# Kernel optimization log

Measured on AMD Instinct MI355X. Metric: run time of the kernel, lower is better.

The kernel has to match this reference:

```python
import jax, jax.numpy as jnp
import numpy as np

EMB = 2048
N_HEADS = 16
HEAD_DIM = EMB // N_HEADS
ROPE_BASE = 10000.0


def _rope_cos_sin(seq_len, head_dim, dtype):
    inv_freq = 1.0 / (ROPE_BASE ** (jnp.arange(0, head_dim, 2, dtype=jnp.float32) / head_dim))
    t = jnp.arange(seq_len, dtype=jnp.float32)
    freqs = jnp.einsum('s,d->sd', t, inv_freq)          # [S, head_dim/2]
    emb = jnp.concatenate([freqs, freqs], axis=-1)       # [S, head_dim]
    return jnp.cos(emb).astype(dtype), jnp.sin(emb).astype(dtype)


def _rotate_half(x):
    x1, x2 = jnp.split(x, 2, axis=-1)
    return jnp.concatenate([-x2, x1], axis=-1)


def _apply_rope(x, cos, sin):
    # x: [B, H, S, D]; cos/sin: [S, D]
    return x * cos[None, None, :, :] + _rotate_half(x) * sin[None, None, :, :]


def setup_inputs() -> dict:
    key = jax.random.key(0)
    k1, k2, k3 = jax.random.split(key, 3)
    B, S = 4, 2048
    x = jax.random.normal(k1, (B, S, EMB), dtype=jnp.float32)
    # Additive causal mask: 0 on/below diagonal, -1e9 above.
    causal = jnp.triu(jnp.full((S, S), -1e9, dtype=jnp.float32), k=1)
    att_mask = causal[None, None, :, :]
    Wqkv = jax.random.normal(k2, (3 * EMB, EMB), dtype=jnp.float32) * (EMB ** -0.5)
    Wout = jax.random.normal(k3, (EMB, EMB), dtype=jnp.float32) * (EMB ** -0.5)
    return {"x": x, "att_mask": att_mask, "Wqkv": Wqkv, "Wout": Wout}


def reference(x, att_mask, Wqkv, Wout):
    B, S, E = x.shape
    qkv = jnp.einsum('bse,fe->bsf', x, Wqkv)             # [B, S, 3E]
    q, k, v = jnp.split(qkv, 3, axis=-1)
    def to_heads(t):
        return t.reshape(B, S, N_HEADS, HEAD_DIM).transpose(0, 2, 1, 3)  # [B,H,S,D]
    q, k, v = to_heads(q), to_heads(k), to_heads(v)
    cos, sin = _rope_cos_sin(S, HEAD_DIM, x.dtype)
    q = _apply_rope(q, cos, sin)
    k = _apply_rope(k, cos, sin)
    scaling = HEAD_DIM ** -0.5
    dots = jnp.einsum('bhqd,bhkd->bhqk', q, k) * scaling
    dots = dots + att_mask
    attn = jax.nn.softmax(dots, axis=-1)
    out = jnp.einsum('bhqk,bhkd->bhqd', attn, v)         # [B,H,S,D]
    out = out.transpose(0, 2, 1, 3).reshape(B, S, E)
    return jnp.einsum('bse,fe->bsf', out, Wout)
```

## Files before the change

### kernel.cpp

```cpp
#include <hip/hip_runtime.h>
#include <stdint.h>

typedef __attribute__((ext_vector_type(8))) short short8_t;
typedef __attribute__((ext_vector_type(4))) float f32x4;

__device__ __forceinline__ short f2bf(float f) {
  union { float f; uint32_t u; } v; v.f = f;
  uint32_t r = v.u + 0x7FFFu + ((v.u >> 16) & 1u);
  return (short)(r >> 16);
}
__device__ __forceinline__ float bf2f(short s) {
  union { uint32_t u; float f; } v; v.u = ((uint32_t)(uint16_t)s) << 16; return v.f;
}
__device__ __forceinline__ void gld16(const void* g, void* l) {
  __builtin_amdgcn_global_load_lds((const __attribute__((address_space(1))) void*)g,
                                   (__attribute__((address_space(3))) void*)l, 16, 0, 0);
}

__global__ __launch_bounds__(256) void conv_kernel(const float* __restrict__ in,
                                                   short* __restrict__ out, int n4) {
  int i = blockIdx.x * 256 + threadIdx.x;
  const int stride = gridDim.x * 256;
  for (; i < n4; i += stride) {
    float4 v = reinterpret_cast<const float4*>(in)[i];
    short4 o;
    o.x = f2bf(v.x); o.y = f2bf(v.y); o.z = f2bf(v.z); o.w = f2bf(v.w);
    reinterpret_cast<short4*>(out)[i] = o;
  }
}

__device__ __forceinline__ void storeC(float* C, size_t i, float v) { C[i] = v; }
__device__ __forceinline__ void storeC(short* C, size_t i, float v) { C[i] = f2bf(v); }

template <typename OT>
__global__ __launch_bounds__(512, 2) void gemm8p(const short* __restrict__ A,
                                                 const short* __restrict__ B,
                                                 OT* __restrict__ C, int M, int N, int K,
                                                 int nbx) {
  __shared__ __align__(16) short lds[65536];
  const int tid = threadIdx.x, lane = tid & 63, w = tid >> 6;
  const int wr = w >> 2, wc = w & 3;
  const int c = lane & 15, g4 = lane >> 4;
  const int lin = (blockIdx.x & 7) * ((int)gridDim.x >> 3) + ((int)blockIdx.x >> 3);
  const int bx = lin % nbx, by = lin / nbx;
  const size_t m0 = (size_t)by * 256, n0 = (size_t)bx * 256;
  const size_t Kb = (size_t)K * 2;
  const char* Ab = (const char*)A + m0 * Kb;
  const char* Bb = (const char*)B + n0 * Kb;
  const char* aq[2];
  const char* bq[2];
#pragma unroll
  for (int i = 0; i < 2; ++i) {
    const size_t ro = (size_t)((i * 8 + w) * 16 + c) * Kb + g4 * 16;
    aq[i] = Ab + ro;
    bq[i] = Bb + ro;
  }
  char* alds = (char*)lds;
  const int aoff = wr * 8192 + lane * 16;
  const int boff = 65536 + wc * 4096 + lane * 16;
  f32x4 acc[8][4] = {};
  const int NT = K >> 6, NIT = NT >> 1;

#define STAGE(q, srcoff, ldsbase)                                  \
  gld16((q)[0] + (srcoff), alds + (ldsbase) + (w << 10));          \
  gld16((q)[1] + (srcoff), alds + (ldsbase) + ((8 + w) << 10))

  STAGE(aq, 0, 0);
  STAGE(bq, 0, 65536);
  STAGE(aq, 64, 16384);
  STAGE(bq, 64, 81920);
  STAGE(aq, 128, 32768);
  STAGE(bq, 128, 98304);
  asm volatile("s_waitcnt vmcnt(0)" ::: "memory");
  asm volatile("s_barrier" ::: "memory");

  short8_t af[4], bfr[4];

#define RD_A(mi, OFF) \
  asm volatile("ds_read_b128 %0, %1 offset:%c2" : "=v"(af[mi]) : "v"(aoff), "i"(OFF))
#define RD_B(ni, OFF) \
  asm volatile("ds_read_b128 %0, %1 offset:%c2" : "=v"(bfr[ni]) : "v"(boff), "i"(OFF))

#define MFMA16(MQ)                                                                       \
  __builtin_amdgcn_s_setprio(1);                                                         \
  _Pragma("unroll") for (int mi = 0; mi < 4; ++mi) {                                     \
    _Pragma("unroll") for (int n = 0; n < 4; ++n)                                        \
      acc[(MQ)*4 + mi][n] =                                                              \
          __builtin_amdgcn_mfma_f32_16x16x32_bf16(af[mi], bfr[n], acc[(MQ)*4 + mi][n],   \
                                                  0, 0, 0);                              \
  }                                                                                      \
  __builtin_amdgcn_s_setprio(0)

#define PH_EVEN(BSEL, KS, q, srcoff, sbase)                        \
  RD_B(0, (BSEL) + (KS)*16384 + 0);                                \
  RD_B(1, (BSEL) + (KS)*16384 + 1024);                             \
  RD_B(2, (BSEL) + (KS)*16384 + 2048);                             \
  RD_B(3, (BSEL) + (KS)*16384 + 3072);                             \
  RD_A(0, (BSEL) + (KS)*16384 + 0 * 1024);                         \
  RD_A(1, (BSEL) + (KS)*16384 + 1 * 1024);                         \
  RD_A(2, (BSEL) + (KS)*16384 + 2 * 1024);                         \
  RD_A(3, (BSEL) + (KS)*16384 + 3 * 1024);                         \
  STAGE(q, srcoff, sbase);                                         \
  asm volatile("s_barrier" ::: "memory");                          \
  asm volatile("s_waitcnt lgkmcnt(0)" ::: "memory");               \
  __builtin_amdgcn_sched_barrier(0);                               \
  MFMA16(0);                                                       \
  asm volatile("s_barrier" ::: "memory")

#define PH_ODD(BSEL, KS, q, srcoff, sbase)                         \
  RD_A(0, (BSEL) + (KS)*16384 + 4 * 1024);                         \
  RD_A(1, (BSEL) + (KS)*16384 + 5 * 1024);                         \
  RD_A(2, (BSEL) + (KS)*16384 + 6 * 1024);                         \
  RD_A(3, (BSEL) + (KS)*16384 + 7 * 1024);                         \
  STAGE(q, srcoff, sbase);                                         \
  asm volatile("s_barrier" ::: "memory");                          \
  asm volatile("s_waitcnt lgkmcnt(0)" ::: "memory");               \
  __builtin_amdgcn_sched_barrier(0);                               \
  MFMA16(1);                                                       \
  asm volatile("s_waitcnt vmcnt(8)" ::: "memory");                 \
  asm volatile("s_barrier" ::: "memory")

  for (int it = 0; it < NIT; ++it) {
    const int T = it << 1;
    const int t1 = (T + 1) << 7;
    const int t2 = (T + 2 < NT ? T + 2 : NT - 1) << 7;
    const int t3 = (T + 3 < NT ? T + 3 : NT - 1) << 7;
    PH_EVEN(0, 0, aq, t1 + 64, 49152);
    PH_ODD (0, 0, bq, t1 + 64, 114688);
    PH_EVEN(0, 1, aq, t2, 0);
    PH_ODD (0, 1, bq, t2, 65536);
    PH_EVEN(32768, 0, aq, t2 + 64, 16384);
    PH_ODD (32768, 0, bq, t2 + 64, 81920);
    PH_EVEN(32768, 1, aq, t3, 32768);
    PH_ODD (32768, 1, bq, t3, 98304);
  }
#undef PH_EVEN
#undef PH_ODD
#undef MFMA16
#undef RD_A
#undef RD_B
#undef STAGE

#pragma unroll
  for (int m = 0; m < 8; ++m)
#pragma unroll
    for (int n = 0; n < 4; ++n) {
      const size_t col = n0 + wc * 64 + n * 16 + c;
      const size_t rb = m0 + wr * 128 + m * 16 + g4 * 4;
#pragma unroll
      for (int r = 0; r < 4; ++r) storeC(C, (rb + r) * (size_t)N + col, acc[m][n][r]);
    }
}

__global__ __launch_bounds__(256) void rope_kernel(short* __restrict__ qkv) {
  const int g = blockIdx.x * 256 + threadIdx.x;
  const int jg = g & 7;
  const int h = (g >> 3) & 15;
  const int bs = g >> 7;
  const int s = bs & 2047;
  const size_t base = (size_t)bs * 6144 + 2048 + h * 128 + jg * 8;
  short8_t lo = *(short8_t*)&qkv[base];
  short8_t hi = *(short8_t*)&qkv[base + 64];
  short8_t olo, ohi;
#pragma unroll
  for (int t = 0; t < 8; ++t) {
    const int j = jg * 8 + t;
    const float inv = exp2f((float)j * -0.20762050593046f);
    float sn, cn;
    sincosf((float)s * inv, &sn, &cn);
    const float a = bf2f(lo[t]), b = bf2f(hi[t]);
    olo[t] = f2bf(a * cn - b * sn);
    ohi[t] = f2bf(b * cn + a * sn);
  }
  *(short8_t*)&qkv[base] = olo;
  *(short8_t*)&qkv[base + 64] = ohi;
}

__global__ __launch_bounds__(256) void vt_kernel(const short* __restrict__ qkv,
                                                 short* __restrict__ vt) {
  __shared__ __align__(16) short Vl[64][128];
  const int g = blockIdx.x;
  const int st = g & 31, bh = g >> 5;
  const int h = bh & 15, b = bh >> 4;
  const int t = threadIdx.x;
  const int s0 = st * 64;
#pragma unroll
  for (int p = 0; p < 4; ++p) {
    const int idx = p * 256 + t;
    const int row = idx >> 4, c16 = idx & 15;
    short8_t v = *(const short8_t*)&qkv[(size_t)(b * 2048 + s0 + row) * 6144 + 4096 + h * 128 + c16 * 8];
    *(short8_t*)&Vl[row][c16 * 8] = v;
  }
  __syncthreads();
  const size_t obase = ((size_t)(b * 16 + h) * 128) * 2048;
#pragma unroll
  for (int i = 0; i < 8; ++i) {
    const int idx = t * 8 + i;
    const int d = idx >> 4, sq = idx & 15;
    short4 o;
    o.x = Vl[sq * 4 + 0][d];
    o.y = Vl[sq * 4 + 1][d];
    o.z = Vl[sq * 4 + 2][d];
    o.w = Vl[sq * 4 + 3][d];
    *(short4*)&vt[obase + (size_t)d * 2048 + s0 + sq * 4] = o;
  }
}

__global__ __launch_bounds__(256) void attn_kernel(const short* __restrict__ qkv,
                                                   const short* __restrict__ vt,
                                                   short* __restrict__ o) {
  __shared__ __align__(16) short Kl[2][64 * 128];
  __shared__ __align__(16) short Vl[2][128 * 64];
  __shared__ __align__(16) short Pl[4][16 * 72];
  const int tid = threadIdx.x, lane = tid & 63, w = tid >> 6;
  const int c = lane & 15, g4 = lane >> 4;
  const int blk = blockIdx.x;
  const int xcd = blk & 7;
  const int l = blk >> 3;
  const int bh = xcd * 8 + (l >> 5);
  const int h = bh & 15, b = bh >> 4;
  const int q0 = (31 - (l & 31)) * 64;
  const int srow = q0 + w * 16 + c;

  short8_t qf[4];
  {
    const size_t qr = ((size_t)b * 2048 + srow) * 6144 + h * 128;
    float fl[4][8];
#pragma unroll
    for (int dc = 0; dc < 4; ++dc) {
      short8_t rawv = *(const short8_t*)&qkv[qr + dc * 32 + g4 * 8];
#pragma unroll
      for (int t = 0; t < 8; ++t) fl[dc][t] = bf2f(rawv[t]);
    }
#pragma unroll
    for (int pd = 0; pd < 2; ++pd)
#pragma unroll
      for (int t = 0; t < 8; ++t) {
        const int j = pd * 32 + g4 * 8 + t;
        const float inv = exp2f((float)j * -0.20762050593046f);
        float sn, cn;
        sincosf((float)srow * inv, &sn, &cn);
        const float a = fl[pd][t], bb = fl[pd + 2][t];
        fl[pd][t] = a * cn - bb * sn;
        fl[pd + 2][t] = bb * cn + a * sn;
      }
#pragma unroll
    for (int dc = 0; dc < 4; ++dc) {
      short8_t q8;
#pragma unroll
      for (int t = 0; t < 8; ++t) q8[t] = f2bf(fl[dc][t]);
      qf[dc] = q8;
    }
  }

  f32x4 acc_o[8] = {};
  float rs[4] = {0.f, 0.f, 0.f, 0.f};
  const float scale2 = 0.12751875222364685f;
  const char* Kbase = (const char*)qkv + ((size_t)b * 2048 * 6144 + 2048 + h * 128) * 2;
  const char* Vbase = (const char*)vt + ((size_t)(b * 16 + h) * 128 * 2048) * 2;

  const char* kq[4];
  const char* vq[4];
#pragma unroll
  for (int i = 0; i < 4; ++i) {
    const int L = ((w * 4 + i) << 10) + lane * 16;
    {
      const int row = L >> 8, inner = L & 255;
      kq[i] = Kbase + (size_t)row * 12288 + (inner ^ ((row & 7) << 4));
    }
    {
      const int row = L >> 7, inner = L & 127;
      vq[i] = Vbase + (size_t)row * 4096 + (inner ^ ((row & 7) << 4));
    }
  }
  auto stage = [&](int buf, int kv0) {
#pragma unroll
    for (int i = 0; i < 4; ++i) {
      gld16(kq[i] + (size_t)kv0 * 12288, (char*)Kl + (buf << 14) + ((w * 4 + i) << 10));
      gld16(vq[i] + (size_t)kv0 * 2, (char*)Vl + (buf << 14) + ((w * 4 + i) << 10));
    }
  };

  stage(0, 0);
  __syncthreads();
  int cur = 0;
  for (int kv0 = 0; kv0 <= q0; kv0 += 64) {
    if (kv0 + 64 <= q0) stage(cur ^ 1, kv0 + 64);
    const char* Kb = (const char*)Kl + (cur << 14);
    const char* Vb = (const char*)Vl + (cur << 14);
    const bool diag = (kv0 == q0);
    float p[4][4];
#pragma unroll
    for (int kt = 0; kt < 4; ++kt) {
      f32x4 s4 = {};
      const int krow = kt * 16 + c;
      __builtin_amdgcn_s_setprio(1);
#pragma unroll
      for (int dc = 0; dc < 4; ++dc) {
        const int inner = (dc * 64 + g4 * 16) ^ ((krow & 7) << 4);
        short8_t kf = *(const short8_t*)(Kb + krow * 256 + inner);
        s4 = __builtin_amdgcn_mfma_f32_16x16x32_bf16(qf[dc], kf, s4, 0, 0, 0);
      }
      __builtin_amdgcn_s_setprio(0);
#pragma unroll
      for (int r = 0; r < 4; ++r) {
        float v = s4[r] * scale2 - 8.0f;
        if (diag) {
          const int kc = kv0 + kt * 16 + c;
          const int qr2 = q0 + w * 16 + g4 * 4 + r;
          if (kc > qr2) v = -1e30f;
        }
        const float pe = exp2f(v);
        p[kt][r] = pe;
        rs[r] += pe;
      }
    }
#pragma unroll
    for (int kt = 0; kt < 4; ++kt)
#pragma unroll
      for (int r = 0; r < 4; r += 2) {
        uint32_t pk;
        asm("v_cvt_pk_bf16_f32 %0, %1, %2" : "=v"(pk) : "v"(p[kt][r]), "v"(p[kt][r + 1]));
        Pl[w][(g4 * 4 + r) * 72 + kt * 16 + c] = (short)(pk & 0xffffu);
        Pl[w][(g4 * 4 + r + 1) * 72 + kt * 16 + c] = (short)(pk >> 16);
      }
#pragma unroll
    for (int kk = 0; kk < 2; ++kk) {
      short8_t pf = *(const short8_t*)&Pl[w][c * 72 + kk * 32 + g4 * 8];
      __builtin_amdgcn_s_setprio(1);
#pragma unroll
      for (int dt = 0; dt < 8; ++dt) {
        const int vrow = dt * 16 + c;
        const int inner = (kk * 64 + g4 * 16) ^ ((vrow & 7) << 4);
        short8_t vf = *(const short8_t*)(Vb + vrow * 128 + inner);
        acc_o[dt] = __builtin_amdgcn_mfma_f32_16x16x32_bf16(pf, vf, acc_o[dt], 0, 0, 0);
      }
      __builtin_amdgcn_s_setprio(0);
    }
    __syncthreads();
    cur ^= 1;
  }
#pragma unroll
  for (int off = 1; off < 16; off <<= 1)
#pragma unroll
    for (int r = 0; r < 4; ++r) rs[r] += __shfl_xor(rs[r], off);
  const size_t ob = ((size_t)b * 2048 + q0 + w * 16 + g4 * 4) * 2048 + h * 128;
#pragma unroll
  for (int dt = 0; dt < 8; ++dt)
#pragma unroll
    for (int r = 0; r < 4; ++r)
      o[ob + (size_t)r * 2048 + dt * 16 + c] = f2bf(acc_o[dt][r] / rs[r]);
}

extern "C" void kernel_launch(void* const* d_in, const int* in_sizes, int n_in,
                              void* d_out, int out_size, void* d_ws, size_t ws_size,
                              hipStream_t stream) {
  const float* x = (const float*)d_in[0];
  const float* Wqkv = (const float*)d_in[2];
  const float* Wout = (const float*)d_in[3];
  float* out = (float*)d_out;
  char* ws = (char*)d_ws;
  short* xb   = (short*)ws;
  short* wqb  = (short*)(ws + 33554432ull);
  short* qkv  = (short*)(ws + 58720256ull);
  short* vt   = (short*)(ws + 159383552ull);
  short* attno = xb;
  short* woutb = wqb;

  conv_kernel<<<2048, 256, 0, stream>>>(x, xb, 16777216 / 4);
  conv_kernel<<<2048, 256, 0, stream>>>(Wqkv, wqb, 12582912 / 4);
  gemm8p<short><<<768, 512, 0, stream>>>(xb, wqb, qkv, 8192, 6144, 2048, 24);
  conv_kernel<<<2048, 256, 0, stream>>>(Wout, woutb, 4194304 / 4);
  rope_kernel<<<4096, 256, 0, stream>>>(qkv);
  vt_kernel<<<2048, 256, 0, stream>>>(qkv, vt);
  attn_kernel<<<2048, 256, 0, stream>>>(qkv, vt, attno);
  gemm8p<float><<<256, 512, 0, stream>>>(attno, woutb, out, 8192, 2048, 2048, 8);
}
```

Measured before the change: 535.9 us.

## Double-buffer LDS fragment registers to prefetch next phase during MFMA

Adds two register sets for the A and B fragments in the GEMM main loop. Each phase now issues the LDS reads for the next phase before running its own MFMAs, and waits only on partial lgkmcnt counts. One barrier per phase is removed. The aim is to hide LDS read latency behind matrix math, at the cost of more VGPRs and tighter correctness requirements on the waitcnt/barrier ordering against async global-to-LDS staging.

```diff
diff --git a/kernel.cpp b/kernel.cpp
--- a/kernel.cpp
+++ b/kernel.cpp
@@ -61,6 +61,8 @@
   f32x4 acc[8][4] = {};
   const int NT = K >> 6, NIT = NT >> 1;
 
+  short8_t af[2][4], bfr[2][4];
+
 #define STAGE(q, srcoff, ldsbase)                                  \
   gld16((q)[0] + (srcoff), alds + (ldsbase) + (w << 10));          \
   gld16((q)[1] + (srcoff), alds + (ldsbase) + ((8 + w) << 10))
@@ -74,69 +76,73 @@
   asm volatile("s_waitcnt vmcnt(0)" ::: "memory");
   asm volatile("s_barrier" ::: "memory");
 
-  short8_t af[4], bfr[4];
-
-#define RD_A(mi, OFF) \
-  asm volatile("ds_read_b128 %0, %1 offset:%c2" : "=v"(af[mi]) : "v"(aoff), "i"(OFF))
-#define RD_B(ni, OFF) \
-  asm volatile("ds_read_b128 %0, %1 offset:%c2" : "=v"(bfr[ni]) : "v"(boff), "i"(OFF))
-
-#define MFMA16(MQ)                                                                       \
+#define RD_A(S, mi, OFF) \
+  asm volatile("ds_read_b128 %0, %1 offset:%c2" : "=v"(af[S][mi]) : "v"(aoff), "i"(OFF))
+#define RD_B(S, ni, OFF) \
+  asm volatile("ds_read_b128 %0, %1 offset:%c2" : "=v"(bfr[S][ni]) : "v"(boff), "i"(OFF))
+
+#define PREF_A(S, BSEL, KS, MQ)                           \
+  RD_A(S, 0, (BSEL) + (KS)*16384 + ((MQ)*4 + 0) * 1024);  \
+  RD_A(S, 1, (BSEL) + (KS)*16384 + ((MQ)*4 + 1) * 1024);  \
+  RD_A(S, 2, (BSEL) + (KS)*16384 + ((MQ)*4 + 2) * 1024);  \
+  RD_A(S, 3, (BSEL) + (KS)*16384 + ((MQ)*4 + 3) * 1024)
+
+#define PREF_B(S, BSEL, KS)                  \
+  RD_B(S, 0, (BSEL) + (KS)*16384 + 0);       \
+  RD_B(S, 1, (BSEL) + (KS)*16384 + 1024);    \
+  RD_B(S, 2, (BSEL) + (KS)*16384 + 2048);    \
+  RD_B(S, 3, (BSEL) + (KS)*16384 + 3072)
+
+#define MFMA16(AS, BS, MQ)                                                               \
   __builtin_amdgcn_s_setprio(1);                                                         \
   _Pragma("unroll") for (int mi = 0; mi < 4; ++mi) {                                     \
     _Pragma("unroll") for (int n = 0; n < 4; ++n)                                        \
-      acc[(MQ)*4 + mi][n] =                                                              \
-          __builtin_amdgcn_mfma_f32_16x16x32_bf16(af[mi], bfr[n], acc[(MQ)*4 + mi][n],   \
-                                                  0, 0, 0);                              \
+      acc[(MQ)*4 + mi][n] = __builtin_amdgcn_mfma_f32_16x16x32_bf16(                     \
+          af[AS][mi], bfr[BS][n], acc[(MQ)*4 + mi][n], 0, 0, 0);                         \
   }                                                                                      \
   __builtin_amdgcn_s_setprio(0)
 
-#define PH_EVEN(BSEL, KS, q, srcoff, sbase)                        \
-  RD_B(0, (BSEL) + (KS)*16384 + 0);                                \
-  RD_B(1, (BSEL) + (KS)*16384 + 1024);                             \
-  RD_B(2, (BSEL) + (KS)*16384 + 2048);                             \
-  RD_B(3, (BSEL) + (KS)*16384 + 3072);                             \
-  RD_A(0, (BSEL) + (KS)*16384 + 0 * 1024);                         \
-  RD_A(1, (BSEL) + (KS)*16384 + 1 * 1024);                         \
-  RD_A(2, (BSEL) + (KS)*16384 + 2 * 1024);                         \
-  RD_A(3, (BSEL) + (KS)*16384 + 3 * 1024);                         \
+#define PHASE_E(AS, BS, PBSEL, PKS, q, srcoff, sbase)              \
+  PREF_A(AS ^ 1, PBSEL, PKS, 1);                                   \
   STAGE(q, srcoff, sbase);                                         \
-  asm volatile("s_barrier" ::: "memory");                          \
-  asm volatile("s_waitcnt lgkmcnt(0)" ::: "memory");               \
+  asm volatile("s_waitcnt lgkmcnt(4)" ::: "memory");               \
   __builtin_amdgcn_sched_barrier(0);                               \
-  MFMA16(0);                                                       \
+  MFMA16(AS, BS, 0);                                               \
+  asm volatile("s_waitcnt vmcnt(6)" ::: "memory");                 \
   asm volatile("s_barrier" ::: "memory")
 
-#define PH_ODD(BSEL, KS, q, srcoff, sbase)                         \
-  RD_A(0, (BSEL) + (KS)*16384 + 4 * 1024);                         \
-  RD_A(1, (BSEL) + (KS)*16384 + 5 * 1024);                         \
-  RD_A(2, (BSEL) + (KS)*16384 + 6 * 1024);                         \
-  RD_A(3, (BSEL) + (KS)*16384 + 7 * 1024);                         \
+#define PHASE_O(AS, BS, PBSEL, PKS, q, srcoff, sbase)              \
+  PREF_B(BS ^ 1, PBSEL, PKS);                                      \
+  PREF_A(AS ^ 1, PBSEL, PKS, 0);                                   \
   STAGE(q, srcoff, sbase);                                         \
-  asm volatile("s_barrier" ::: "memory");                          \
-  asm volatile("s_waitcnt lgkmcnt(0)" ::: "memory");               \
+  asm volatile("s_waitcnt lgkmcnt(8)" ::: "memory");               \
   __builtin_amdgcn_sched_barrier(0);                               \
-  MFMA16(1);                                                       \
+  MFMA16(AS, BS, 1);                                               \
   asm volatile("s_waitcnt vmcnt(8)" ::: "memory");                 \
   asm volatile("s_barrier" ::: "memory")
+
+  PREF_B(0, 0, 0);
+  PREF_A(0, 0, 0, 0);
 
   for (int it = 0; it < NIT; ++it) {
     const int T = it << 1;
     const int t1 = (T + 1) << 7;
     const int t2 = (T + 2 < NT ? T + 2 : NT - 1) << 7;
     const int t3 = (T + 3 < NT ? T + 3 : NT - 1) << 7;
-    PH_EVEN(0, 0, aq, t1 + 64, 49152);
-    PH_ODD (0, 0, bq, t1 + 64, 114688);
-    PH_EVEN(0, 1, aq, t2, 0);
-    PH_ODD (0, 1, bq, t2, 65536);
-    PH_EVEN(32768, 0, aq, t2 + 64, 16384);
-    PH_ODD (32768, 0, bq, t2 + 64, 81920);
-    PH_EVEN(32768, 1, aq, t3, 32768);
-    PH_ODD (32768, 1, bq, t3, 98304);
-  }
-#undef PH_EVEN
-#undef PH_ODD
+    PHASE_E(0, 0, 0, 0,      aq, t1 + 64, 49152);
+    PHASE_O(1, 0, 0, 1,      bq, t1 + 64, 114688);
+    PHASE_E(0, 1, 0, 1,      aq, t2, 0);
+    PHASE_O(1, 1, 32768, 0,  bq, t2, 65536);
+    PHASE_E(0, 0, 32768, 0,  aq, t2 + 64, 16384);
+    PHASE_O(1, 0, 32768, 1,  bq, t2 + 64, 81920);
+    PHASE_E(0, 1, 32768, 1,  aq, t3, 32768);
+    PHASE_O(1, 1, 0, 0,      bq, t3, 98304);
+  }
+#undef PHASE_E
+#undef PHASE_O
 #undef MFMA16
+#undef PREF_A
+#undef PREF_B
 #undef RD_A
 #undef RD_B
 #undef STAGE
```

Measured after the change: 535.9 us. No clear change (-0.0%).
